# Kernel optimization log

Hardware: AMD Instinct MI355X
Metric: run time of the kernel (lower is better)

Reference implementation:

```python
import jax, jax.numpy as jnp
import numpy as np

HEADS = 16
HEAD_DIM = 64
EMBED = HEADS * HEAD_DIM  # 1024
B, S = 2, 2048


def setup_inputs() -> dict:
    key = jax.random.key(0)
    ks = jax.random.split(key, 9)
    return {
        "value": jax.random.normal(ks[0], (B, S, EMBED), dtype=jnp.float32),
        "key": jax.random.normal(ks[1], (B, S, EMBED), dtype=jnp.float32),
        "query": jax.random.normal(ks[2], (B, S, EMBED), dtype=jnp.float32),
        "mask": jax.random.randint(ks[3], (B, 1, S, S), 0, 2, dtype=jnp.int32),
        "Wq": jax.random.normal(ks[4], (HEAD_DIM, HEAD_DIM), dtype=jnp.float32) * 0.02,
        "Wk": jax.random.normal(ks[5], (HEAD_DIM, HEAD_DIM), dtype=jnp.float32) * 0.02,
        "Wv": jax.random.normal(ks[6], (HEAD_DIM, HEAD_DIM), dtype=jnp.float32) * 0.02,
        "Wo": jax.random.normal(ks[7], (EMBED, EMBED), dtype=jnp.float32) * 0.02,
        "bo": jnp.zeros((EMBED,), dtype=jnp.float32),
    }


def reference(value, key, query, mask, Wq, Wk, Wv, Wo, bo):
    N, Lv = value.shape[0], value.shape[1]
    Lk, Lq = key.shape[1], query.shape[1]
    # Faithful to original: plain reshape (N, heads, len, head_dim), NOT transpose.
    v = value.reshape(N, HEADS, Lv, HEAD_DIM)
    k = key.reshape(N, HEADS, Lk, HEAD_DIM)
    q = query.reshape(N, HEADS, Lq, HEAD_DIM)
    # Per-head Linear (no bias): x @ W.T
    V = jnp.einsum('bhld,ed->bhle', v, Wv)
    K = jnp.einsum('bhld,ed->bhle', k, Wk)
    Q = jnp.einsum('bhld,ed->bhle', q, Wq)
    score = jnp.einsum('bhqd,bhkd->bhqk', Q, K)  # [B,H,Sq,Sk]
    score = jnp.where(mask == 0, jnp.float32(-1e20), score)
    # Faithful quirk: scale by sqrt(embed_size), not sqrt(head_dim)
    scale = jnp.float32(EMBED ** 0.5)
    attn = jax.nn.softmax(score / scale, axis=3)
    out = jnp.einsum('bhqk,bhkd->bhqd', attn, V).reshape(N, Lq, HEADS * HEAD_DIM)
    return out @ Wo.T + bo
```

## Files before the change

kernel.cpp:

```cpp
#include <hip/hip_runtime.h>
#include <hip/hip_bf16.h>
#include <cstdint>
#include <cstddef>

#define S_LEN 2048
#define N_HEADS 16
#define HD 64
#define EMB 1024
#define N_BATCH 2
#define N_BH (N_BATCH * N_HEADS)

typedef __attribute__((ext_vector_type(4))) float f32x4;
typedef __attribute__((ext_vector_type(8))) short short8;
typedef __attribute__((ext_vector_type(8))) _Float16 half8;
typedef __attribute__((ext_vector_type(2))) _Float16 half2v;

__device__ __forceinline__ f32x4 mfma16h(half8 a, half8 b, f32x4 c) {
    return __builtin_amdgcn_mfma_f32_16x16x32_f16(a, b, c, 0, 0, 0);
}

__device__ __forceinline__ unsigned pkh(float a, float b) {
    return __builtin_bit_cast(unsigned, __builtin_amdgcn_cvt_pkrtz(a, b));
}

#if __has_builtin(__builtin_amdgcn_exp2f)
__device__ __forceinline__ float fast_exp2(float x) { return __builtin_amdgcn_exp2f(x); }
#else
__device__ __forceinline__ float fast_exp2(float x) { return exp2f(x); }
#endif

__global__ __launch_bounds__(256) void prep_kernel(
    const float* __restrict__ q_in, const float* __restrict__ k_in,
    const float* __restrict__ v_in,
    const float* __restrict__ Wq, const float* __restrict__ Wk,
    const float* __restrict__ Wv, const float* __restrict__ Wo,
    const int* __restrict__ mask,
    short* __restrict__ Qb, short* __restrict__ Kb, short* __restrict__ Vt,
    short* __restrict__ Woh, unsigned long long* __restrict__ bits) {
    __shared__ short Al[64 * 72];
    __shared__ short Wl[64 * 72];
    __shared__ short Ol[64 * 72];
    int bx = blockIdx.x;
    int t = threadIdx.x;

    if (bx >= 3072) {
        if (bx < 11264) {
            int wid = ((bx - 3072) * 256 + t) >> 6;
            int lane = t & 63;
            const int* src = mask + (size_t)wid * 256 + lane;
            unsigned long long w0 = __ballot(src[0] != 0);
            unsigned long long w1 = __ballot(src[64] != 0);
            unsigned long long w2 = __ballot(src[128] != 0);
            unsigned long long w3 = __ballot(src[192] != 0);
            if (lane == 0) {
                unsigned long long* dst = bits + (size_t)wid * 4;
                dst[0] = w0; dst[1] = w1; dst[2] = w2; dst[3] = w3;
            }
        } else {
            int i = (bx - 11264) * 256 + t;
            f32x4 a = reinterpret_cast<const f32x4*>(Wo)[i * 2];
            f32x4 b = reinterpret_cast<const f32x4*>(Wo)[i * 2 + 1];
            uint4 u = { pkh(a.x, a.y), pkh(a.z, a.w), pkh(b.x, b.y), pkh(b.z, b.w) };
            reinterpret_cast<uint4*>(Woh)[i] = u;
        }
        return;
    }

    int rt = bx & 31;
    int bh = (bx >> 5) & 31;
    int tz = bx >> 10;
    const float* src = (tz == 0 ? q_in : tz == 1 ? k_in : v_in)
                       + (size_t)bh * S_LEN * HD + (size_t)rt * 64 * HD;
    const float* W = (tz == 0 ? Wq : tz == 1 ? Wk : Wv);

#pragma unroll
    for (int r = 0; r < 4; r++) {
        int f4 = t + 256 * r;
        int row = f4 >> 4;
        int c4 = (f4 & 15) * 4;
        f32x4 a = reinterpret_cast<const f32x4*>(src)[f4];
        uint2 ua = { pkh(a.x, a.y), pkh(a.z, a.w) };
        *reinterpret_cast<uint2*>(&Al[row * 72 + c4]) = ua;
        f32x4 w = reinterpret_cast<const f32x4*>(W)[f4];
        uint2 uw = { pkh(w.x, w.y), pkh(w.z, w.w) };
        *reinterpret_cast<uint2*>(&Wl[row * 72 + c4]) = uw;
    }
    __syncthreads();

    int wave = t >> 6, lane = t & 63, quad = lane >> 4, col = lane & 15;
    half8 a0 = *reinterpret_cast<const half8*>(&Al[(wave * 16 + col) * 72 + quad * 8]);
    half8 a1 = *reinterpret_cast<const half8*>(&Al[(wave * 16 + col) * 72 + 32 + quad * 8]);

    const float C1 = 0.04508422002777448f;
    float scl = (tz == 0) ? C1 : 1.0f;

    f32x4 acc[4];
#pragma unroll
    for (int jt = 0; jt < 4; jt++) {
        half8 b0 = *reinterpret_cast<const half8*>(&Wl[(jt * 16 + col) * 72 + quad * 8]);
        half8 b1 = *reinterpret_cast<const half8*>(&Wl[(jt * 16 + col) * 72 + 32 + quad * 8]);
        f32x4 c = {0.f, 0.f, 0.f, 0.f};
        c = mfma16h(a0, b0, c);
        c = mfma16h(a1, b1, c);
        acc[jt] = c;
    }
    __syncthreads();

    if (tz < 2) {
#pragma unroll
        for (int jt = 0; jt < 4; jt++)
#pragma unroll
            for (int i = 0; i < 4; i++)
                Ol[(wave * 16 + quad * 4 + i) * 72 + jt * 16 + col] =
                    __builtin_bit_cast(short, (_Float16)(acc[jt][i] * scl));
        __syncthreads();
        short* dst = (tz == 0 ? Qb : Kb) + (size_t)bh * S_LEN * HD + (size_t)rt * 64 * HD;
        int row = t >> 2, ck = (t & 3) * 16;
        short8 o0 = *reinterpret_cast<const short8*>(&Ol[row * 72 + ck]);
        short8 o1 = *reinterpret_cast<const short8*>(&Ol[row * 72 + ck + 8]);
        *reinterpret_cast<short8*>(&dst[row * 64 + ck]) = o0;
        *reinterpret_cast<short8*>(&dst[row * 64 + ck + 8]) = o1;
    } else {
#pragma unroll
        for (int jt = 0; jt < 4; jt++)
#pragma unroll
            for (int i = 0; i < 4; i++)
                Ol[(jt * 16 + col) * 72 + wave * 16 + quad * 4 + i] =
                    __builtin_bit_cast(short, (_Float16)acc[jt][i]);
        __syncthreads();
        short* dst = Vt + (size_t)bh * HD * S_LEN + rt * 64;
        int d = t >> 2, ck = (t & 3) * 16;
        short8 o0 = *reinterpret_cast<const short8*>(&Ol[d * 72 + ck]);
        short8 o1 = *reinterpret_cast<const short8*>(&Ol[d * 72 + ck + 8]);
        *reinterpret_cast<short8*>(&dst[(size_t)d * S_LEN + ck]) = o0;
        *reinterpret_cast<short8*>(&dst[(size_t)d * S_LEN + ck + 8]) = o1;
    }
}

__global__ __launch_bounds__(512, 4) void attn_kernel(
    const short* __restrict__ Qb, const short* __restrict__ Kb,
    const short* __restrict__ Vt, const unsigned long long* __restrict__ mbits,
    short* __restrict__ Xb) {
    int qt = blockIdx.x;
    int bh = blockIdx.y;
    int b = bh >> 4;
    int t = threadIdx.x, wave = t >> 6, lane = t & 63, quad = lane >> 4, col = lane & 15;

    __shared__ short Ks[64 * 64];
    __shared__ short Vs[64 * 64];
    __shared__ short Pl[8][16 * 72];
    short* Pw = &Pl[wave][0];

    const short* Qh = Qb + (size_t)bh * S_LEN * HD;
    const short* Kh = Kb + (size_t)bh * S_LEN * HD;
    const short* Vh = Vt + (size_t)bh * HD * S_LEN;
    int q0w = qt * 128 + wave * 16;
    int q = q0w + col;

    half8 qf0 = *reinterpret_cast<const half8*>(&Qh[(size_t)q * HD + quad * 8]);
    half8 qf1 = *reinterpret_cast<const half8*>(&Qh[(size_t)q * HD + 32 + quad * 8]);
    const unsigned long long* mrow = mbits + (size_t)(b * S_LEN + q) * 32;

    int r0 = t >> 3, cc = t & 7;
    int dst0 = r0 * 64 + ((cc ^ (r0 & 7)) * 8);
    const short* kg0 = Kh + r0 * HD + cc * 8;
    const short* vg0 = Vh + (size_t)r0 * S_LEN + cc * 8;

    short8 pk0 = *reinterpret_cast<const short8*>(kg0);
    short8 pv0 = *reinterpret_cast<const short8*>(vg0);
    *reinterpret_cast<short8*>(&Ks[dst0]) = pk0;
    *reinterpret_cast<short8*>(&Vs[dst0]) = pv0;
    __syncthreads();

    unsigned bs[4];
#pragma unroll
    for (int i = 0; i < 4; i++) bs[i] = 1u << (quad * 4 + i);
    half8 ones = { (_Float16)1.f, (_Float16)1.f, (_Float16)1.f, (_Float16)1.f,
                   (_Float16)1.f, (_Float16)1.f, (_Float16)1.f, (_Float16)1.f };

    int sw = quad ^ (col & 7);
    unsigned long long mw = mrow[0];

    f32x4 o[4];
    f32x4 l = {0.f, 0.f, 0.f, 0.f};
#pragma unroll
    for (int dt = 0; dt < 4; dt++) o[dt] = (f32x4){0.f, 0.f, 0.f, 0.f};

    for (int kt = 0; kt < 32; kt++) {
        unsigned long long mw_n;
        if (kt < 31) {
            pk0 = *reinterpret_cast<const short8*>(kg0 + (kt + 1) * 4096);
            pv0 = *reinterpret_cast<const short8*>(vg0 + (kt + 1) * 64);
            mw_n = mrow[kt + 1];
        }
        f32x4 s[4];
#pragma unroll
        for (int mt = 0; mt < 4; mt++) {
            const short* kbase = &Ks[(mt * 16 + col) * 64];
            half8 ka0 = *reinterpret_cast<const half8*>(&kbase[sw * 8]);
            half8 ka1 = *reinterpret_cast<const half8*>(&kbase[(sw ^ 4) * 8]);
            f32x4 c = {0.f, 0.f, 0.f, 0.f};
            c = mfma16h(ka0, qf0, c);
            c = mfma16h(ka1, qf1, c);
            s[mt] = c;
        }
#pragma unroll
        for (int mt = 0; mt < 4; mt++) {
            unsigned g = (unsigned)(mw >> (mt * 16));
            float p0 = fast_exp2((g & bs[0]) ? s[mt][0] : -200.0f);
            float p1 = fast_exp2((g & bs[1]) ? s[mt][1] : -200.0f);
            float p2 = fast_exp2((g & bs[2]) ? s[mt][2] : -200.0f);
            float p3 = fast_exp2((g & bs[3]) ? s[mt][3] : -200.0f);
            uint2 dw = { pkh(p0, p1), pkh(p2, p3) };
            *reinterpret_cast<uint2*>(&Pw[col * 72 + mt * 16 + quad * 4]) = dw;
        }
#pragma unroll
        for (int c = 0; c < 2; c++) {
            half8 pb = *reinterpret_cast<const half8*>(&Pw[col * 72 + c * 32 + quad * 8]);
            l = mfma16h(ones, pb, l);
#pragma unroll
            for (int dt = 0; dt < 4; dt++) {
                half8 va = *reinterpret_cast<const half8*>(
                    &Vs[(dt * 16 + col) * 64 + (((c * 4 + quad) ^ (col & 7)) * 8)]);
                o[dt] = mfma16h(va, pb, o[dt]);
            }
        }
        __syncthreads();
        if (kt < 31) {
            *reinterpret_cast<short8*>(&Ks[dst0]) = pk0;
            *reinterpret_cast<short8*>(&Vs[dst0]) = pv0;
            mw = mw_n;
            __syncthreads();
        }
    }

    float inv = 1.0f / l[0];
#pragma unroll
    for (int dt = 0; dt < 4; dt++) {
        uint2 dw = { pkh(o[dt][0] * inv, o[dt][1] * inv),
                     pkh(o[dt][2] * inv, o[dt][3] * inv) };
        *reinterpret_cast<uint2*>(&Pw[col * 72 + dt * 16 + quad * 4]) = dw;
    }
    int rr = lane >> 2, ck = (lane & 3) * 16;
    short8 x0 = *reinterpret_cast<const short8*>(&Pw[rr * 72 + ck]);
    short8 x1 = *reinterpret_cast<const short8*>(&Pw[rr * 72 + ck + 8]);
    short* Xrow = Xb + (size_t)bh * S_LEN * HD + (size_t)(q0w + rr) * HD;
    *reinterpret_cast<short8*>(&Xrow[ck]) = x0;
    *reinterpret_cast<short8*>(&Xrow[ck + 8]) = x1;
}

__global__ __launch_bounds__(256, 4) void final_kernel(
    const short* __restrict__ Xb, const short* __restrict__ Woh,
    const float* __restrict__ bo, float* __restrict__ out) {
    int nb = blockIdx.x;
    int mb = blockIdx.y;
    int t = threadIdx.x, wave = t >> 6, lane = t & 63, quad = lane >> 4, col = lane & 15;
    __shared__ short Xs[64 * 64];
    __shared__ short Ws[64 * 64];
    __shared__ float Olds[64 * 68];

    int m0 = mb * 64, n0 = nb * 64;
    int r0 = t >> 3, r1 = (t + 256) >> 3, cc = t & 7;
    int dst0 = r0 * 64 + ((cc ^ (r0 & 7)) * 8);
    int dst1 = r1 * 64 + ((cc ^ (r1 & 7)) * 8);
    const short* xg0 = Xb + (size_t)(m0 + r0) * EMB + cc * 8;
    const short* xg1 = Xb + (size_t)(m0 + r1) * EMB + cc * 8;
    const short* wg0 = Woh + (size_t)(n0 + r0) * EMB + cc * 8;
    const short* wg1 = Woh + (size_t)(n0 + r1) * EMB + cc * 8;

    short8 px0 = *reinterpret_cast<const short8*>(xg0);
    short8 px1 = *reinterpret_cast<const short8*>(xg1);
    short8 pw0 = *reinterpret_cast<const short8*>(wg0);
    short8 pw1 = *reinterpret_cast<const short8*>(wg1);
    *reinterpret_cast<short8*>(&Xs[dst0]) = px0;
    *reinterpret_cast<short8*>(&Xs[dst1]) = px1;
    *reinterpret_cast<short8*>(&Ws[dst0]) = pw0;
    *reinterpret_cast<short8*>(&Ws[dst1]) = pw1;
    __syncthreads();

    int sw = quad ^ (col & 7);
    f32x4 acc[4];
#pragma unroll
    for (int jt = 0; jt < 4; jt++) acc[jt] = (f32x4){0.f, 0.f, 0.f, 0.f};

    for (int s = 0; s < 16; s++) {
        if (s < 15) {
            px0 = *reinterpret_cast<const short8*>(xg0 + (s + 1) * 64);
            px1 = *reinterpret_cast<const short8*>(xg1 + (s + 1) * 64);
            pw0 = *reinterpret_cast<const short8*>(wg0 + (s + 1) * 64);
            pw1 = *reinterpret_cast<const short8*>(wg1 + (s + 1) * 64);
        }
        const short* arow = &Xs[(wave * 16 + col) * 64];
        half8 a0 = *reinterpret_cast<const half8*>(&arow[sw * 8]);
        half8 a1 = *reinterpret_cast<const half8*>(&arow[(sw ^ 4) * 8]);
#pragma unroll
        for (int jt = 0; jt < 4; jt++) {
            const short* brow = &Ws[(jt * 16 + col) * 64];
            half8 b0 = *reinterpret_cast<const half8*>(&brow[sw * 8]);
            half8 b1 = *reinterpret_cast<const half8*>(&brow[(sw ^ 4) * 8]);
            acc[jt] = mfma16h(a0, b0, acc[jt]);
            acc[jt] = mfma16h(a1, b1, acc[jt]);
        }
        __syncthreads();
        if (s < 15) {
            *reinterpret_cast<short8*>(&Xs[dst0]) = px0;
            *reinterpret_cast<short8*>(&Xs[dst1]) = px1;
            *reinterpret_cast<short8*>(&Ws[dst0]) = pw0;
            *reinterpret_cast<short8*>(&Ws[dst1]) = pw1;
            __syncthreads();
        }
    }

#pragma unroll
    for (int jt = 0; jt < 4; jt++)
#pragma unroll
        for (int i = 0; i < 4; i++)
            Olds[(wave * 16 + quad * 4 + i) * 68 + jt * 16 + col] = acc[jt][i];
    __syncthreads();
    int row = t >> 2, ck = (t & 3) * 16;
#pragma unroll
    for (int u = 0; u < 4; u++) {
        f32x4 v = *reinterpret_cast<const f32x4*>(&Olds[row * 68 + ck + u * 4]);
        f32x4 bb = *reinterpret_cast<const f32x4*>(&bo[n0 + ck + u * 4]);
        v.x += bb.x; v.y += bb.y; v.z += bb.z; v.w += bb.w;
        *reinterpret_cast<f32x4*>(&out[(size_t)(m0 + row) * EMB + n0 + ck + u * 4]) = v;
    }
}

extern "C" void kernel_launch(void* const* d_in, const int* in_sizes, int n_in,
                              void* d_out, int out_size, void* d_ws, size_t ws_size,
                              hipStream_t stream) {
    const float* value = (const float*)d_in[0];
    const float* key_  = (const float*)d_in[1];
    const float* query = (const float*)d_in[2];
    const int*   mask  = (const int*)d_in[3];
    const float* Wq = (const float*)d_in[4];
    const float* Wk = (const float*)d_in[5];
    const float* Wv = (const float*)d_in[6];
    const float* Wo = (const float*)d_in[7];
    const float* bo = (const float*)d_in[8];
    float* out = (float*)d_out;

    char* ws = (char*)d_ws;
    short* Qb  = (short*)(ws);
    short* Kb  = (short*)(ws + (size_t)8  * 1048576);
    short* Vt  = (short*)(ws + (size_t)16 * 1048576);
    short* Xb  = (short*)(ws + (size_t)24 * 1048576);
    short* Woh = (short*)(ws + (size_t)32 * 1048576);
    unsigned long long* mbits =
        (unsigned long long*)(ws + (size_t)34 * 1048576);

    prep_kernel<<<dim3(3072 + 8192 + 512), dim3(256), 0, stream>>>(
        query, key_, value, Wq, Wk, Wv, Wo, mask, Qb, Kb, Vt, Woh, mbits);
    attn_kernel<<<dim3(S_LEN / 128, N_BH), dim3(512), 0, stream>>>(Qb, Kb, Vt, mbits, Xb);
    final_kernel<<<dim3(EMB / 64, (N_BATCH * S_LEN) / 64), dim3(256), 0, stream>>>(
        Xb, Woh, bo, out);
}
```

Measured before the change: 204.7 us.

## Give each attention wave two query tiles and enlarge output GEMM tiles

```diff
diff --git a/kernel.cpp b/kernel.cpp
--- a/kernel.cpp
+++ b/kernel.cpp
@@ -13,7 +13,6 @@
 typedef __attribute__((ext_vector_type(4))) float f32x4;
 typedef __attribute__((ext_vector_type(8))) short short8;
 typedef __attribute__((ext_vector_type(8))) _Float16 half8;
-typedef __attribute__((ext_vector_type(2))) _Float16 half2v;
 
 __device__ __forceinline__ f32x4 mfma16h(half8 a, half8 b, f32x4 c) {
     return __builtin_amdgcn_mfma_f32_16x16x32_f16(a, b, c, 0, 0, 0);
@@ -44,20 +43,18 @@
     int t = threadIdx.x;
 
     if (bx >= 3072) {
-        if (bx < 11264) {
-            int wid = ((bx - 3072) * 256 + t) >> 6;
+        if (bx < 5120) {
+            int gw = (bx - 3072) * 4 + (t >> 6);
             int lane = t & 63;
-            const int* src = mask + (size_t)wid * 256 + lane;
-            unsigned long long w0 = __ballot(src[0] != 0);
-            unsigned long long w1 = __ballot(src[64] != 0);
-            unsigned long long w2 = __ballot(src[128] != 0);
-            unsigned long long w3 = __ballot(src[192] != 0);
-            if (lane == 0) {
-                unsigned long long* dst = bits + (size_t)wid * 4;
-                dst[0] = w0; dst[1] = w1; dst[2] = w2; dst[3] = w3;
+            const int* src = mask + (size_t)gw * 1024 + lane;
+            unsigned long long* dst = bits + (size_t)gw * 16;
+#pragma unroll
+            for (int r = 0; r < 16; r++) {
+                unsigned long long w = __ballot(src[r * 64] != 0);
+                if (lane == 0) dst[r] = w;
             }
         } else {
-            int i = (bx - 11264) * 256 + t;
+            int i = (bx - 5120) * 256 + t;
             f32x4 a = reinterpret_cast<const f32x4*>(Wo)[i * 2];
             f32x4 b = reinterpret_cast<const f32x4*>(Wo)[i * 2 + 1];
             uint4 u = { pkh(a.x, a.y), pkh(a.z, a.w), pkh(b.x, b.y), pkh(b.z, b.w) };
@@ -137,7 +134,7 @@
     }
 }
 
-__global__ __launch_bounds__(512, 4) void attn_kernel(
+__global__ __launch_bounds__(256, 4) void attn_kernel(
     const short* __restrict__ Qb, const short* __restrict__ Kb,
     const short* __restrict__ Vt, const unsigned long long* __restrict__ mbits,
     short* __restrict__ Xb) {
@@ -149,118 +146,159 @@
     __shared__ short Ks[64 * 64];
     __shared__ short Vs[64 * 64];
     __shared__ short Pl[8][16 * 72];
-    short* Pw = &Pl[wave][0];
+    short* PwA = &Pl[wave * 2][0];
+    short* PwB = &Pl[wave * 2 + 1][0];
 
     const short* Qh = Qb + (size_t)bh * S_LEN * HD;
     const short* Kh = Kb + (size_t)bh * S_LEN * HD;
     const short* Vh = Vt + (size_t)bh * HD * S_LEN;
-    int q0w = qt * 128 + wave * 16;
-    int q = q0w + col;
-
-    half8 qf0 = *reinterpret_cast<const half8*>(&Qh[(size_t)q * HD + quad * 8]);
-    half8 qf1 = *reinterpret_cast<const half8*>(&Qh[(size_t)q * HD + 32 + quad * 8]);
-    const unsigned long long* mrow = mbits + (size_t)(b * S_LEN + q) * 32;
-
-    int r0 = t >> 3, cc = t & 7;
+    int qb0 = qt * 128 + wave * 32;
+    int qA = qb0 + col, qB = qb0 + 16 + col;
+
+    half8 qA0 = *reinterpret_cast<const half8*>(&Qh[(size_t)qA * HD + quad * 8]);
+    half8 qA1 = *reinterpret_cast<const half8*>(&Qh[(size_t)qA * HD + 32 + quad * 8]);
+    half8 qB0 = *reinterpret_cast<const half8*>(&Qh[(size_t)qB * HD + quad * 8]);
+    half8 qB1 = *reinterpret_cast<const half8*>(&Qh[(size_t)qB * HD + 32 + quad * 8]);
+    const unsigned long long* mrowA = mbits + (size_t)(b * S_LEN + qA) * 32;
+    const unsigned long long* mrowB = mbits + (size_t)(b * S_LEN + qB) * 32;
+
+    int r0 = t >> 3, r1 = r0 + 32, cc = t & 7;
     int dst0 = r0 * 64 + ((cc ^ (r0 & 7)) * 8);
+    int dst1 = r1 * 64 + ((cc ^ (r1 & 7)) * 8);
     const short* kg0 = Kh + r0 * HD + cc * 8;
+    const short* kg1 = Kh + r1 * HD + cc * 8;
     const short* vg0 = Vh + (size_t)r0 * S_LEN + cc * 8;
+    const short* vg1 = Vh + (size_t)r1 * S_LEN + cc * 8;
 
     short8 pk0 = *reinterpret_cast<const short8*>(kg0);
+    short8 pk1 = *reinterpret_cast<const short8*>(kg1);
     short8 pv0 = *reinterpret_cast<const short8*>(vg0);
+    short8 pv1 = *reinterpret_cast<const short8*>(vg1);
     *reinterpret_cast<short8*>(&Ks[dst0]) = pk0;
+    *reinterpret_cast<short8*>(&Ks[dst1]) = pk1;
     *reinterpret_cast<short8*>(&Vs[dst0]) = pv0;
+    *reinterpret_cast<short8*>(&Vs[dst1]) = pv1;
     __syncthreads();
 
     unsigned bs[4];
 #pragma unroll
     for (int i = 0; i < 4; i++) bs[i] = 1u << (quad * 4 + i);
-    half8 ones = { (_Float16)1.f, (_Float16)1.f, (_Float16)1.f, (_Float16)1.f,
-                   (_Float16)1.f, (_Float16)1.f, (_Float16)1.f, (_Float16)1.f };
-
     int sw = quad ^ (col & 7);
-    unsigned long long mw = mrow[0];
-
-    f32x4 o[4];
-    f32x4 l = {0.f, 0.f, 0.f, 0.f};
-#pragma unroll
-    for (int dt = 0; dt < 4; dt++) o[dt] = (f32x4){0.f, 0.f, 0.f, 0.f};
+    unsigned long long mwA = mrowA[0], mwB = mrowB[0];
+
+    f32x4 o[2][4];
+    float lA = 0.f, lB = 0.f;
+#pragma unroll
+    for (int u = 0; u < 2; u++)
+#pragma unroll
+        for (int dt = 0; dt < 4; dt++) o[u][dt] = (f32x4){0.f, 0.f, 0.f, 0.f};
 
     for (int kt = 0; kt < 32; kt++) {
-        unsigned long long mw_n;
+        unsigned long long mwA_n, mwB_n;
         if (kt < 31) {
             pk0 = *reinterpret_cast<const short8*>(kg0 + (kt + 1) * 4096);
+            pk1 = *reinterpret_cast<const short8*>(kg1 + (kt + 1) * 4096);
             pv0 = *reinterpret_cast<const short8*>(vg0 + (kt + 1) * 64);
-            mw_n = mrow[kt + 1];
-        }
-        f32x4 s[4];
+            pv1 = *reinterpret_cast<const short8*>(vg1 + (kt + 1) * 64);
+            mwA_n = mrowA[kt + 1];
+            mwB_n = mrowB[kt + 1];
+        }
+        f32x4 sA[4], sB[4];
 #pragma unroll
         for (int mt = 0; mt < 4; mt++) {
             const short* kbase = &Ks[(mt * 16 + col) * 64];
             half8 ka0 = *reinterpret_cast<const half8*>(&kbase[sw * 8]);
             half8 ka1 = *reinterpret_cast<const half8*>(&kbase[(sw ^ 4) * 8]);
-            f32x4 c = {0.f, 0.f, 0.f, 0.f};
-            c = mfma16h(ka0, qf0, c);
-            c = mfma16h(ka1, qf1, c);
-            s[mt] = c;
+            f32x4 cA = {0.f, 0.f, 0.f, 0.f};
+            cA = mfma16h(ka0, qA0, cA);
+            cA = mfma16h(ka1, qA1, cA);
+            sA[mt] = cA;
+            f32x4 cB = {0.f, 0.f, 0.f, 0.f};
+            cB = mfma16h(ka0, qB0, cB);
+            cB = mfma16h(ka1, qB1, cB);
+            sB[mt] = cB;
         }
 #pragma unroll
         for (int mt = 0; mt < 4; mt++) {
-            unsigned g = (unsigned)(mw >> (mt * 16));
-            float p0 = fast_exp2((g & bs[0]) ? s[mt][0] : -200.0f);
-            float p1 = fast_exp2((g & bs[1]) ? s[mt][1] : -200.0f);
-            float p2 = fast_exp2((g & bs[2]) ? s[mt][2] : -200.0f);
-            float p3 = fast_exp2((g & bs[3]) ? s[mt][3] : -200.0f);
-            uint2 dw = { pkh(p0, p1), pkh(p2, p3) };
-            *reinterpret_cast<uint2*>(&Pw[col * 72 + mt * 16 + quad * 4]) = dw;
+            unsigned gA = (unsigned)(mwA >> (mt * 16));
+            float a0 = fast_exp2((gA & bs[0]) ? sA[mt][0] : -200.0f);
+            float a1 = fast_exp2((gA & bs[1]) ? sA[mt][1] : -200.0f);
+            float a2 = fast_exp2((gA & bs[2]) ? sA[mt][2] : -200.0f);
+            float a3 = fast_exp2((gA & bs[3]) ? sA[mt][3] : -200.0f);
+            lA += (a0 + a1) + (a2 + a3);
+            uint2 dwA = { pkh(a0, a1), pkh(a2, a3) };
+            *reinterpret_cast<uint2*>(&PwA[col * 72 + mt * 16 + quad * 4]) = dwA;
+            unsigned gB = (unsigned)(mwB >> (mt * 16));
+            float b0 = fast_exp2((gB & bs[0]) ? sB[mt][0] : -200.0f);
+            float b1 = fast_exp2((gB & bs[1]) ? sB[mt][1] : -200.0f);
+            float b2 = fast_exp2((gB & bs[2]) ? sB[mt][2] : -200.0f);
+            float b3 = fast_exp2((gB & bs[3]) ? sB[mt][3] : -200.0f);
+            lB += (b0 + b1) + (b2 + b3);
+            uint2 dwB = { pkh(b0, b1), pkh(b2, b3) };
+            *reinterpret_cast<uint2*>(&PwB[col * 72 + mt * 16 + quad * 4]) = dwB;
         }
 #pragma unroll
         for (int c = 0; c < 2; c++) {
-            half8 pb = *reinterpret_cast<const half8*>(&Pw[col * 72 + c * 32 + quad * 8]);
-            l = mfma16h(ones, pb, l);
+            half8 pbA = *reinterpret_cast<const half8*>(&PwA[col * 72 + c * 32 + quad * 8]);
+            half8 pbB = *reinterpret_cast<const half8*>(&PwB[col * 72 + c * 32 + quad * 8]);
 #pragma unroll
             for (int dt = 0; dt < 4; dt++) {
                 half8 va = *reinterpret_cast<const half8*>(
                     &Vs[(dt * 16 + col) * 64 + (((c * 4 + quad) ^ (col & 7)) * 8)]);
-                o[dt] = mfma16h(va, pb, o[dt]);
+                o[0][dt] = mfma16h(va, pbA, o[0][dt]);
+                o[1][dt] = mfma16h(va, pbB, o[1][dt]);
             }
         }
         __syncthreads();
         if (kt < 31) {
             *reinterpret_cast<short8*>(&Ks[dst0]) = pk0;
+            *reinterpret_cast<short8*>(&Ks[dst1]) = pk1;
             *reinterpret_cast<short8*>(&Vs[dst0]) = pv0;
-            mw = mw_n;
+            *reinterpret_cast<short8*>(&Vs[dst1]) = pv1;
+            mwA = mwA_n;
+            mwB = mwB_n;
             __syncthreads();
         }
     }
 
-    float inv = 1.0f / l[0];
+    lA += __shfl_xor(lA, 16); lA += __shfl_xor(lA, 32);
+    lB += __shfl_xor(lB, 16); lB += __shfl_xor(lB, 32);
+    float invA = 1.0f / lA, invB = 1.0f / lB;
+
 #pragma unroll
     for (int dt = 0; dt < 4; dt++) {
-        uint2 dw = { pkh(o[dt][0] * inv, o[dt][1] * inv),
-                     pkh(o[dt][2] * inv, o[dt][3] * inv) };
-        *reinterpret_cast<uint2*>(&Pw[col * 72 + dt * 16 + quad * 4]) = dw;
+        uint2 dwA = { pkh(o[0][dt][0] * invA, o[0][dt][1] * invA),
+                      pkh(o[0][dt][2] * invA, o[0][dt][3] * invA) };
+        *reinterpret_cast<uint2*>(&PwA[col * 72 + dt * 16 + quad * 4]) = dwA;
+        uint2 dwB = { pkh(o[1][dt][0] * invB, o[1][dt][1] * invB),
+                      pkh(o[1][dt][2] * invB, o[1][dt][3] * invB) };
+        *reinterpret_cast<uint2*>(&PwB[col * 72 + dt * 16 + quad * 4]) = dwB;
     }
     int rr = lane >> 2, ck = (lane & 3) * 16;
-    short8 x0 = *reinterpret_cast<const short8*>(&Pw[rr * 72 + ck]);
-    short8 x1 = *reinterpret_cast<const short8*>(&Pw[rr * 72 + ck + 8]);
-    short* Xrow = Xb + (size_t)bh * S_LEN * HD + (size_t)(q0w + rr) * HD;
-    *reinterpret_cast<short8*>(&Xrow[ck]) = x0;
-    *reinterpret_cast<short8*>(&Xrow[ck + 8]) = x1;
-}
-
-__global__ __launch_bounds__(256, 4) void final_kernel(
+    short8 x0 = *reinterpret_cast<const short8*>(&PwA[rr * 72 + ck]);
+    short8 x1 = *reinterpret_cast<const short8*>(&PwA[rr * 72 + ck + 8]);
+    short* XrowA = Xb + (size_t)bh * S_LEN * HD + (size_t)(qb0 + rr) * HD;
+    *reinterpret_cast<short8*>(&XrowA[ck]) = x0;
+    *reinterpret_cast<short8*>(&XrowA[ck + 8]) = x1;
+    short8 y0 = *reinterpret_cast<const short8*>(&PwB[rr * 72 + ck]);
+    short8 y1 = *reinterpret_cast<const short8*>(&PwB[rr * 72 + ck + 8]);
+    short* XrowB = Xb + (size_t)bh * S_LEN * HD + (size_t)(qb0 + 16 + rr) * HD;
+    *reinterpret_cast<short8*>(&XrowB[ck]) = y0;
+    *reinterpret_cast<short8*>(&XrowB[ck + 8]) = y1;
+}
+
+__global__ __launch_bounds__(512, 2) void final_kernel(
     const short* __restrict__ Xb, const short* __restrict__ Woh,
     const float* __restrict__ bo, float* __restrict__ out) {
     int nb = blockIdx.x;
     int mb = blockIdx.y;
     int t = threadIdx.x, wave = t >> 6, lane = t & 63, quad = lane >> 4, col = lane & 15;
-    __shared__ short Xs[64 * 64];
-    __shared__ short Ws[64 * 64];
-    __shared__ float Olds[64 * 68];
-
-    int m0 = mb * 64, n0 = nb * 64;
-    int r0 = t >> 3, r1 = (t + 256) >> 3, cc = t & 7;
+    int mw2 = wave >> 1, nw = wave & 1;
+    __shared__ short Xs[128 * 64];
+    __shared__ short Ws[128 * 64];
+
+    int m0 = mb * 128, n0 = nb * 128;
+    int r0 = t >> 3, r1 = r0 + 64, cc = t & 7;
     int dst0 = r0 * 64 + ((cc ^ (r0 & 7)) * 8);
     int dst1 = r1 * 64 + ((cc ^ (r1 & 7)) * 8);
     const short* xg0 = Xb + (size_t)(m0 + r0) * EMB + cc * 8;
@@ -278,10 +316,11 @@
     *reinterpret_cast<short8*>(&Ws[dst1]) = pw1;
     __syncthreads();
 
-    int sw = quad ^ (col & 7);
-    f32x4 acc[4];
-#pragma unroll
-    for (int jt = 0; jt < 4; jt++) acc[jt] = (f32x4){0.f, 0.f, 0.f, 0.f};
+    f32x4 acc[2][4];
+#pragma unroll
+    for (int mu = 0; mu < 2; mu++)
+#pragma unroll
+        for (int nf = 0; nf < 4; nf++) acc[mu][nf] = (f32x4){0.f, 0.f, 0.f, 0.f};
 
     for (int s = 0; s < 16; s++) {
         if (s < 15) {
@@ -290,16 +329,23 @@
             pw0 = *reinterpret_cast<const short8*>(wg0 + (s + 1) * 64);
             pw1 = *reinterpret_cast<const short8*>(wg1 + (s + 1) * 64);
         }
-        const short* arow = &Xs[(wave * 16 + col) * 64];
-        half8 a0 = *reinterpret_cast<const half8*>(&arow[sw * 8]);
-        half8 a1 = *reinterpret_cast<const half8*>(&arow[(sw ^ 4) * 8]);
-#pragma unroll
-        for (int jt = 0; jt < 4; jt++) {
-            const short* brow = &Ws[(jt * 16 + col) * 64];
-            half8 b0 = *reinterpret_cast<const half8*>(&brow[sw * 8]);
-            half8 b1 = *reinterpret_cast<const half8*>(&brow[(sw ^ 4) * 8]);
-            acc[jt] = mfma16h(a0, b0, acc[jt]);
-            acc[jt] = mfma16h(a1, b1, acc[jt]);
+#pragma unroll
+        for (int k2 = 0; k2 < 2; k2++) {
+            half8 a[2];
+#pragma unroll
+            for (int mu = 0; mu < 2; mu++) {
+                int rl = mw2 * 32 + mu * 16 + col;
+                a[mu] = *reinterpret_cast<const half8*>(
+                    &Xs[rl * 64 + (((k2 * 4 + quad) ^ (rl & 7)) * 8)]);
+            }
+#pragma unroll
+            for (int nf = 0; nf < 4; nf++) {
+                int rl = nw * 64 + nf * 16 + col;
+                half8 bfr = *reinterpret_cast<const half8*>(
+                    &Ws[rl * 64 + (((k2 * 4 + quad) ^ (rl & 7)) * 8)]);
+                acc[0][nf] = mfma16h(a[0], bfr, acc[0][nf]);
+                acc[1][nf] = mfma16h(a[1], bfr, acc[1][nf]);
+            }
         }
         __syncthreads();
         if (s < 15) {
@@ -312,18 +358,16 @@
     }
 
 #pragma unroll
-    for (int jt = 0; jt < 4; jt++)
-#pragma unroll
-        for (int i = 0; i < 4; i++)
-            Olds[(wave * 16 + quad * 4 + i) * 68 + jt * 16 + col] = acc[jt][i];
-    __syncthreads();
-    int row = t >> 2, ck = (t & 3) * 16;
-#pragma unroll
-    for (int u = 0; u < 4; u++) {
-        f32x4 v = *reinterpret_cast<const f32x4*>(&Olds[row * 68 + ck + u * 4]);
-        f32x4 bb = *reinterpret_cast<const f32x4*>(&bo[n0 + ck + u * 4]);
-        v.x += bb.x; v.y += bb.y; v.z += bb.z; v.w += bb.w;
-        *reinterpret_cast<f32x4*>(&out[(size_t)(m0 + row) * EMB + n0 + ck + u * 4]) = v;
+    for (int nf = 0; nf < 4; nf++) {
+        int n = n0 + nw * 64 + nf * 16 + col;
+        float bb = bo[n];
+#pragma unroll
+        for (int mu = 0; mu < 2; mu++) {
+            int row = m0 + mw2 * 32 + mu * 16 + quad * 4;
+#pragma unroll
+            for (int i = 0; i < 4; i++)
+                out[(size_t)(row + i) * EMB + n] = acc[mu][nf][i] + bb;
+        }
     }
 }
 
@@ -350,9 +394,9 @@
     unsigned long long* mbits =
         (unsigned long long*)(ws + (size_t)34 * 1048576);
 
-    prep_kernel<<<dim3(3072 + 8192 + 512), dim3(256), 0, stream>>>(
+    prep_kernel<<<dim3(3072 + 2048 + 512), dim3(256), 0, stream>>>(
         query, key_, value, Wq, Wk, Wv, Wo, mask, Qb, Kb, Vt, Woh, mbits);
-    attn_kernel<<<dim3(S_LEN / 128, N_BH), dim3(512), 0, stream>>>(Qb, Kb, Vt, mbits, Xb);
-    final_kernel<<<dim3(EMB / 64, (N_BATCH * S_LEN) / 64), dim3(256), 0, stream>>>(
+    attn_kernel<<<dim3(S_LEN / 128, N_BH), dim3(256), 0, stream>>>(Qb, Kb, Vt, mbits, Xb);
+    final_kernel<<<dim3(EMB / 128, (N_BATCH * S_LEN) / 128), dim3(512), 0, stream>>>(
         Xb, Woh, bo, out);
 }
```

Measured after the change: 232.0 us. +13.4%, slower.
